# Kernel optimization log

Hardware: AMD Instinct MI355X
Metric: run time of the kernel (lower is better)

## Reference

```python
import jax, jax.numpy as jnp
import numpy as np

B, N, P2, D, L, K = 256, 256, 64, 128, 2, 9  # batch, nodes, patch^2, embed_dim, vig blocks, knn edges
FFN = 4 * D


def _ln(x, g, b, eps=1e-5):
    m = jnp.mean(x, -1, keepdims=True)
    v = jnp.mean((x - m) ** 2, -1, keepdims=True)
    return (x - m) / jnp.sqrt(v + eps) * g + b


def _lrelu(x):
    return jnp.where(x >= 0, x, 0.01 * x)


def _vig_block(x, mask, mf, fc1_w, fc1_b, conv_w, conv_b, fc2_w, fc2_b, f1_w, f1_b, f2_w, f2_b):
    # Grapher: fc1 -> dynamic kNN -> max-relative graph conv -> fc2, residual
    sc = x
    h = x @ fc1_w + fc1_b  # [B,N,D]
    # pairwise squared distances in feature space; masked nodes excluded as neighbors
    x2 = jnp.sum(h * h, -1)
    d2 = x2[:, :, None] + x2[:, None, :] - 2.0 * jnp.einsum('bnd,bmd->bnm', h, h)
    d2 = jnp.where(mask[:, None, :], d2, 1e10)
    _, idx = jax.lax.top_k(-d2, K)  # [B,N,K] nearest-neighbor indices (non-diff)
    Bq, Nq, Dq = h.shape
    hj = jnp.take_along_axis(h, idx.reshape(Bq, Nq * K, 1), axis=1).reshape(Bq, Nq, K, Dq)
    vj = jnp.take_along_axis(mask, idx.reshape(Bq, Nq * K), axis=1).reshape(Bq, Nq, K)
    rel = jnp.where(vj[..., None], hj - h[:, :, None, :], -1e9)
    mrel = jnp.where(vj.any(2)[..., None], rel.max(2), 0.0)  # max-relative aggregation
    h = _lrelu(jnp.concatenate([h, mrel], -1) @ conv_w + conv_b)
    x = (h @ fc2_w + fc2_b) + sc
    # FFN, residual (drop_path = identity at eval)
    sc = x
    x = _lrelu(x @ f1_w + f1_b) @ f2_w + f2_b + sc
    return x * mf


def setup_inputs() -> dict:
    key = jax.random.key(0)
    ks = jax.random.split(key, 32)
    s = 0.02
    d = {
        'nodes_batch': jax.random.normal(ks[0], (B, N, P2), jnp.float32),
        'node_mask': jax.random.randint(ks[1], (B, N), 0, 2) > 0,
        'emb_w1': jax.random.normal(ks[2], (P2, 2 * D), jnp.float32) * s,
        'emb_b1': jnp.zeros((2 * D,), jnp.float32),
        'emb_ln1_g': jnp.ones((2 * D,), jnp.float32),
        'emb_ln1_b': jnp.zeros((2 * D,), jnp.float32),
        'emb_w2': jax.random.normal(ks[3], (2 * D, D), jnp.float32) * s,
        'emb_b2': jnp.zeros((D,), jnp.float32),
        'emb_ln2_g': jnp.ones((D,), jnp.float32),
        'emb_ln2_b': jnp.zeros((D,), jnp.float32),
        'vig_fc1_w': jax.random.normal(ks[4], (L, D, D), jnp.float32) * s,
        'vig_fc1_b': jnp.zeros((L, D), jnp.float32),
        'vig_conv_w': jax.random.normal(ks[5], (L, 2 * D, D), jnp.float32) * s,
        'vig_conv_b': jnp.zeros((L, D), jnp.float32),
        'vig_fc2_w': jax.random.normal(ks[6], (L, D, D), jnp.float32) * s,
        'vig_fc2_b': jnp.zeros((L, D), jnp.float32),
        'vig_ffn1_w': jax.random.normal(ks[7], (L, D, FFN), jnp.float32) * s,
        'vig_ffn1_b': jnp.zeros((L, FFN), jnp.float32),
        'vig_ffn2_w': jax.random.normal(ks[8], (L, FFN, D), jnp.float32) * s,
        'vig_ffn2_b': jnp.zeros((L, D), jnp.float32),
        'out_w1': jax.random.normal(ks[9], (D, 512), jnp.float32) * s,
        'out_b1': jnp.zeros((512,), jnp.float32),
        'out_w2': jax.random.normal(ks[10], (512, 2048), jnp.float32) * s,
        'out_b2': jnp.zeros((2048,), jnp.float32),
    }
    return d


def reference(nodes_batch, node_mask, emb_w1, emb_b1, emb_ln1_g, emb_ln1_b, emb_w2, emb_b2,
              emb_ln2_g, emb_ln2_b, vig_fc1_w, vig_fc1_b, vig_conv_w, vig_conv_b,
              vig_fc2_w, vig_fc2_b, vig_ffn1_w, vig_ffn1_b, vig_ffn2_w, vig_ffn2_b,
              out_w1, out_b1, out_w2, out_b2):
    mf = node_mask[..., None].astype(nodes_batch.dtype)  # [B,N,1]
    # node embed MLP
    x = _lrelu(_ln(nodes_batch @ emb_w1 + emb_b1, emb_ln1_g, emb_ln1_b))
    x = _ln(x @ emb_w2 + emb_b2, emb_ln2_g, emb_ln2_b)
    x = x * mf
    for l in range(L):
        x = _vig_block(x, node_mask, mf,
                       vig_fc1_w[l], vig_fc1_b[l], vig_conv_w[l], vig_conv_b[l],
                       vig_fc2_w[l], vig_fc2_b[l], vig_ffn1_w[l], vig_ffn1_b[l],
                       vig_ffn2_w[l], vig_ffn2_b[l])
    # masked mean pool
    sum_feat = (x * mf).sum(1)
    num_feat = jnp.maximum(mf.sum(1), 1.0)
    g = sum_feat / num_feat
    return _lrelu(g @ out_w1 + out_b1) @ out_w2 + out_b2
```

## Files before the change

### kernel.cpp

```cpp
#include <hip/hip_runtime.h>
#include <cstdint>

#define BB    256
#define NNODE 256
#define PP2   64
#define DD    128
#define LLAY  2
#define KNN   9
#define FFND  512
#define BNROWS (BB*NNODE)

#define LRELU_(v) ((v) >= 0.f ? (v) : 0.01f*(v))

enum { ACT_NONE = 0, ACT_LRELU = 1 };

typedef short  short8_t  __attribute__((ext_vector_type(8)));
typedef float  f32x4     __attribute__((ext_vector_type(4)));
typedef unsigned short us4 __attribute__((ext_vector_type(4)));
typedef unsigned short us8 __attribute__((ext_vector_type(8)));

__device__ inline unsigned short f2bf(float x) {
    unsigned u = __float_as_uint(x);
    unsigned r = (u + 0x7FFFu + ((u >> 16) & 1u)) >> 16;
    return (unsigned short)r;
}
__device__ inline float bf2f(unsigned short h) {
    return __uint_as_float(((unsigned)h) << 16);
}

__device__ inline void gload16(const void* src, void* dst) {
    __builtin_amdgcn_global_load_lds(
        (const __attribute__((address_space(1))) void*)src,
        (__attribute__((address_space(3))) void*)dst, 16, 0, 0);
}

template<int ROWS, int WAVES>
__device__ inline void stage64g(const unsigned short* __restrict__ g, size_t rowbase,
                                int Kel, int k0, unsigned short* lds, int w, int lane)
{
    constexpr int PER = (ROWS*128/1024) / WAVES;
    #pragma unroll
    for (int i = 0; i < PER; ++i) {
        const int inst = w + i*WAVES;
        const unsigned o  = (unsigned)inst*1024u + (unsigned)lane*16u;
        const int      r  = (int)(o >> 7);
        const unsigned cb = o & 127u;
        const unsigned cs = cb ^ ((unsigned)(r & 7) << 4);
        gload16((const char*)(g + (rowbase + (size_t)r)*(size_t)Kel + k0) + cs,
                (char*)lds + (size_t)inst*1024u);
    }
}

__device__ inline short8_t frag64(const unsigned short* lds, int r, int cb) {
    return *reinterpret_cast<const short8_t*>(
        (const char*)lds + (size_t)r*128 + (unsigned)(cb ^ ((r & 7) << 4)));
}

__device__ inline us8 read8sw(const unsigned short* lds, int r, unsigned cb) {
    return *reinterpret_cast<const us8*>(
        (const char*)lds + (size_t)r*128 + (cb ^ ((unsigned)(r & 7) << 4)));
}

__device__ inline unsigned grp16_min_u32(unsigned v) {
    unsigned t;
    t = (unsigned)__builtin_amdgcn_update_dpp(-1, (int)v, 0xB1,  0xF, 0xF, false); v = t < v ? t : v;
    t = (unsigned)__builtin_amdgcn_update_dpp(-1, (int)v, 0x4E,  0xF, 0xF, false); v = t < v ? t : v;
    t = (unsigned)__builtin_amdgcn_update_dpp(-1, (int)v, 0x124, 0xF, 0xF, false); v = t < v ? t : v;
    t = (unsigned)__builtin_amdgcn_update_dpp(-1, (int)v, 0x128, 0xF, 0xF, false); v = t < v ? t : v;
    return v;
}

__device__ inline float dpp_rowsum16(float v) {
    float t;
    t = __uint_as_float((unsigned)__builtin_amdgcn_update_dpp(0, (int)__float_as_uint(v), 0x111, 0xF, 0xF, false)); v += t;
    t = __uint_as_float((unsigned)__builtin_amdgcn_update_dpp(0, (int)__float_as_uint(v), 0x112, 0xF, 0xF, false)); v += t;
    t = __uint_as_float((unsigned)__builtin_amdgcn_update_dpp(0, (int)__float_as_uint(v), 0x114, 0xF, 0xF, false)); v += t;
    t = __uint_as_float((unsigned)__builtin_amdgcn_update_dpp(0, (int)__float_as_uint(v), 0x118, 0xF, 0xF, false)); v += t;
    return v;
}

#define WAITB0  { asm volatile("s_waitcnt vmcnt(0)" ::: "memory");  __builtin_amdgcn_s_barrier(); asm volatile("" ::: "memory"); }
#define WAITB2  { asm volatile("s_waitcnt vmcnt(2)" ::: "memory");  __builtin_amdgcn_s_barrier(); asm volatile("" ::: "memory"); }
#define WAITB3  { asm volatile("s_waitcnt vmcnt(3)" ::: "memory");  __builtin_amdgcn_s_barrier(); asm volatile("" ::: "memory"); }
#define WAITB2L { asm volatile("s_waitcnt vmcnt(2) lgkmcnt(0)" ::: "memory"); __builtin_amdgcn_s_barrier(); asm volatile("" ::: "memory"); }

template<int ACT, bool RES, bool MASK, bool OUTF, bool OUTB, bool OUTS>
__global__ __launch_bounds__(256)
void bgemm_k(const unsigned short* __restrict__ A,
             const unsigned short* __restrict__ W,
             const float* __restrict__ bias,
             const float* __restrict__ resp,
             const int* __restrict__ mask,
             float* __restrict__ Cf, unsigned short* __restrict__ Cb,
             unsigned short* Ohi, unsigned short* Olo,
             int M, int N, int K)
{
    __shared__ __align__(16) unsigned short As[128*64];
    __shared__ __align__(16) unsigned short Bs[128*64];

    const int tid  = threadIdx.x;
    const int lane = tid & 63;
    const int w    = tid >> 6;
    const int wr   = w >> 1, wc = w & 1;
    const int row0 = blockIdx.x * 128;
    const int col0 = blockIdx.y * 128;
    const int l15  = lane & 15;
    const int ko   = lane >> 4;

    f32x4 acc[4][4];
    #pragma unroll
    for (int m = 0; m < 4; ++m)
        #pragma unroll
        for (int n = 0; n < 4; ++n) acc[m][n] = (f32x4){0.f,0.f,0.f,0.f};

    for (int k0 = 0; k0 < K; k0 += 64) {
        stage64g<128,4>(A, (size_t)row0, K, k0, As, w, lane);
        stage64g<128,4>(W, (size_t)col0, K, k0, Bs, w, lane);
        __syncthreads();
        #pragma unroll
        for (int ks = 0; ks < 2; ++ks) {
            short8_t aF[4], bF[4];
            #pragma unroll
            for (int m = 0; m < 4; ++m)
                aF[m] = frag64(As, wr*64 + m*16 + l15, ks*64 + ko*16);
            #pragma unroll
            for (int n = 0; n < 4; ++n)
                bF[n] = frag64(Bs, wc*64 + n*16 + l15, ks*64 + ko*16);
            #pragma unroll
            for (int m = 0; m < 4; ++m)
                #pragma unroll
                for (int n = 0; n < 4; ++n)
                    acc[m][n] = __builtin_amdgcn_mfma_f32_16x16x32_bf16(aF[m], bF[n], acc[m][n], 0, 0, 0);
        }
        __syncthreads();
    }

    #pragma unroll
    for (int m = 0; m < 4; ++m) {
        const int rbase = row0 + wr*64 + m*16 + ko*4;
        #pragma unroll
        for (int n = 0; n < 4; ++n) {
            const int col = col0 + wc*64 + n*16 + l15;
            const float bv = bias[col];
            #pragma unroll
            for (int r = 0; r < 4; ++r) {
                const int row = rbase + r;
                float v = acc[m][n][r] + bv;
                if constexpr (ACT == ACT_LRELU) v = LRELU_(v);
                if constexpr (RES)  v += resp[(size_t)row*N + col];
                if constexpr (MASK) v *= (mask[row] != 0) ? 1.f : 0.f;
                if constexpr (OUTF) Cf[(size_t)row*N + col] = v;
                if constexpr (OUTB) Cb[(size_t)row*N + col] = f2bf(v);
                if constexpr (OUTS) {
                    unsigned short h = f2bf(v);
                    Ohi[(size_t)row*N + col] = h;
                    Olo[(size_t)row*N + col] = f2bf(v - bf2f(h));
                }
            }
        }
    }
}

template<int WR, int WC, bool DO_LRELU, bool MASKMUL, int MODE, bool AF32>
__global__ __launch_bounds__(WR*WC*64)
void bgemm_ln_k(const void* __restrict__ Ap,
                const unsigned short* __restrict__ W,
                const float* __restrict__ bias,
// ... 63 lines not shown
            for (int n = 0; n < 4; ++n)
                bF[n] = frag64(Bs, wc*64 + n*16 + l15, ks*64 + ko*16);
            #pragma unroll
            for (int m = 0; m < 4; ++m)
                #pragma unroll
                for (int n = 0; n < 4; ++n)
                    acc[m][n] = __builtin_amdgcn_mfma_f32_16x16x32_bf16(aF[m], bF[n], acc[m][n], 0, 0, 0);
        }
        __syncthreads();
    }

    float bv[4];
    #pragma unroll
    for (int n = 0; n < 4; ++n) bv[n] = bias[wc*64 + n*16 + l15];
    #pragma unroll
    for (int m = 0; m < 4; ++m)
        #pragma unroll
        for (int n = 0; n < 4; ++n)
            #pragma unroll
            for (int r = 0; r < 4; ++r) acc[m][n][r] += bv[n];

    #pragma unroll
    for (int m = 0; m < 4; ++m) {
        #pragma unroll
        for (int r = 0; r < 4; ++r) {
            float s = acc[m][0][r] + acc[m][1][r] + acc[m][2][r] + acc[m][3][r];
            float q = acc[m][0][r]*acc[m][0][r] + acc[m][1][r]*acc[m][1][r]
                    + acc[m][2][r]*acc[m][2][r] + acc[m][3][r]*acc[m][3][r];
            s = dpp_rowsum16(s);
            q = dpp_rowsum16(q);
            if (l15 == 15) {
                int rl = wr*64 + m*16 + ko*4 + r;
                red_s[wc][rl] = s;
                red_q[wc][rl] = q;
            }
        }
    }
    __syncthreads();
    if (tid < BM) {
        float s = 0.f, q = 0.f;
        #pragma unroll
        for (int c2 = 0; c2 < WC; ++c2) { s += red_s[c2][tid]; q += red_q[c2][tid]; }
        float mu  = s * (1.0f/BN);
        float var = q * (1.0f/BN) - mu*mu;
        mu_l[tid] = mu;
        rs_l[tid] = rsqrtf(fmaxf(var, 0.f) + 1e-5f);
    }
    __syncthreads();

    float gm[4], bt[4];
    #pragma unroll
    for (int n = 0; n < 4; ++n) {
        int col = wc*64 + n*16 + l15;
        gm[n] = gam[col]; bt[n] = bet[col];
    }
    #pragma unroll
    for (int m = 0; m < 4; ++m) {
        #pragma unroll
        for (int r = 0; r < 4; ++r) {
            const int rl  = wr*64 + m*16 + ko*4 + r;
            const int row = row0 + rl;
            const float mu = mu_l[rl], rs = rs_l[rl];
            float mf = 1.f;
            if constexpr (MASKMUL) mf = (mask[row] != 0) ? 1.f : 0.f;
            #pragma unroll
            for (int n = 0; n < 4; ++n) {
                const int col = wc*64 + n*16 + l15;
                float y = (acc[m][n][r] - mu) * rs * gm[n] + bt[n];
                if constexpr (DO_LRELU) y = LRELU_(y);
                if constexpr (MASKMUL)  y *= mf;
                if constexpr (MODE == 1) {
                    ((unsigned short*)outv)[(size_t)row*BN + col] = f2bf(y);
                } else {
                    unsigned short h = f2bf(y);
                    ohi[(size_t)row*BN + col] = h;
                    olo[(size_t)row*BN + col] = f2bf(y - bf2f(h));
                }
            }
        }
    }
}

__global__ __launch_bounds__(1024)
void fc1_dist_topk_gather_k(const unsigned short* __restrict__ xhi,
                            const unsigned short* __restrict__ xlo,
                            const unsigned short* __restrict__ Whi,
                            const unsigned short* __restrict__ Wlo,
                            const float* __restrict__ fc1b,
                            const int* __restrict__ mask,
                            unsigned short* __restrict__ cat)
{
    __shared__ __align__(16) unsigned short BUF[4][NNODE*64];
    __shared__ __align__(16) unsigned short Ws[128*64];
    __shared__ float x2s[NNODE];
    __shared__ unsigned char idx_s[NNODE*KNN];
    __shared__ unsigned char msk_s[NNODE];

    const int b    = blockIdx.x;
    const int tid  = threadIdx.x;
    const int lane = tid & 63;
    const int w    = tid >> 6;
    const int l15  = lane & 15;
    const int g    = lane >> 4;

    const unsigned short* Xhi = xhi + (size_t)b*NNODE*DD;
    const unsigned short* Xlo = xlo + (size_t)b*NNODE*DD;
    const int* mkb = mask + b*NNODE;

    stage64g<NNODE,16>(Xhi, 0, DD, 0,  &BUF[0][0], w, lane);
    stage64g<NNODE,16>(Xhi, 0, DD, 64, &BUF[1][0], w, lane);
    stage64g<NNODE,16>(Xlo, 0, DD, 0,  &BUF[2][0], w, lane);
    stage64g<NNODE,16>(Xlo, 0, DD, 64, &BUF[3][0], w, lane);
    if (tid < NNODE) msk_s[tid] = (mkb[tid] != 0) ? 1 : 0;
    __syncthreads();

    const int arow = w*16 + l15;

    f32x4 hacc[8];
    #pragma unroll
    for (int n = 0; n < 8; ++n) hacc[n] = (f32x4){0.f,0.f,0.f,0.f};

    #pragma unroll
    for (int wp = 0; wp < 4; ++wp) {
        const unsigned short* Wsrc = (wp < 2) ? Whi : Wlo;
        const int kt = wp & 1;
        stage64g<128,16>(Wsrc, 0, DD, kt*64, Ws, w, lane);
        __syncthreads();
        const int nAv = (wp < 2) ? 2 : 1;
        for (int av = 0; av < nAv; ++av) {
            const unsigned short* At = (av == 0) ? &BUF[kt][0] : &BUF[2+kt][0];
            #pragma unroll
            for (int ks = 0; ks < 2; ++ks) {
                short8_t aF = frag64(At, arow, ks*64 + g*16);
                #pragma unroll
                for (int n = 0; n < 8; ++n) {
                    short8_t bF = frag64(Ws, n*16 + l15, ks*64 + g*16);
                    hacc[n] = __builtin_amdgcn_mfma_f32_16x16x32_bf16(aF, bF, hacc[n], 0, 0, 0);
                }
            }
        }
        __syncthreads();
    }

    {
        float qr[4] = {0.f, 0.f, 0.f, 0.f};
        #pragma unroll
        for (int n = 0; n < 8; ++n) {
            const int col = n*16 + l15;
            const float bv = fc1b[col];
            const int kt = col >> 6;
            const unsigned bc = (unsigned)((col & 63) * 2);
            #pragma unroll
            for (int r = 0; r < 4; ++r) {
                const int row = w*16 + g*4 + r;
                float v = hacc[n][r] + bv;
                unsigned short hh = f2bf(v);
                unsigned short hl = f2bf(v - bf2f(hh));
                const unsigned off = (unsigned)(row*128) + (bc ^ ((unsigned)(row & 7) << 4));
                *(unsigned short*)((char*)&BUF[kt][0]   + off) = hh;
                *(unsigned short*)((char*)&BUF[2+kt][0] + off) = hl;
                float vv = bf2f(hh) + bf2f(hl);
                qr[r] += vv*vv;
            }
        }
        #pragma unroll
        for (int r = 0; r < 4; ++r) {
            float q = dpp_rowsum16(qr[r]);
            if (l15 == 15) x2s[w*16 + g*4 + r] = q;
        }
    }
    __syncthreads();

    f32x4 acc[16];
    #pragma unroll
    for (int n = 0; n < 16; ++n) acc[n] = (f32x4){0.f,0.f,0.f,0.f};

    __builtin_amdgcn_s_setprio(1);
    #pragma unroll
    for (int kt = 0; kt < 2; ++kt) {
        #pragma unroll
        for (int ks = 0; ks < 2; ++ks) {
            short8_t aH = frag64(&BUF[kt][0],   arow, ks*64 + g*16);
            short8_t aL = frag64(&BUF[2+kt][0], arow, ks*64 + g*16);
            #pragma unroll
            for (int n = 0; n < 16; ++n) {
                int brow = n*16 + l15;
                short8_t bH = frag64(&BUF[kt][0],   brow, ks*64 + g*16);
                short8_t bL = frag64(&BUF[2+kt][0], brow, ks*64 + g*16);
                acc[n] = __builtin_amdgcn_mfma_f32_16x16x32_bf16(aH, bH, acc[n], 0, 0, 0);
                acc[n] = __builtin_amdgcn_mfma_f32_16x16x32_bf16(aL, bH, acc[n], 0, 0, 0);
                acc[n] = __builtin_amdgcn_mfma_f32_16x16x32_bf16(aH, bL, acc[n], 0, 0, 0);
            }
        }
    }
    __builtin_amdgcn_s_setprio(0);

    float x2c[16]; unsigned mk[16];
    #pragma unroll
    for (int n = 0; n < 16; ++n) {
        int col = n*16 + l15;
        x2c[n] = x2s[col];
        mk[n]  = (unsigned)msk_s[col];
    }

    #pragma unroll
    for (int r = 0; r < 4; ++r) {
        const int rb = w*16 + r;
        if ((msk_s[rb] | msk_s[rb+4] | msk_s[rb+8] | msk_s[rb+12]) == 0) continue;
        const int lrow = w*16 + g*4 + r;
        const float x2r = x2s[lrow];
        unsigned key[16];
        #pragma unroll
        for (int n = 0; n < 16; ++n) {
            float v = x2r + x2c[n] - 2.0f*acc[n][r];
            if (!mk[n]) v = 1e10f;
            unsigned u = __float_as_uint(v);
            u = (u & 0x80000000u) ? ~u : (u | 0x80000000u);
            key[n] = (u & 0xFFFFFF00u) | (unsigned)(n*16 + l15);
        }
        for (int it = 0; it < KNN; ++it) {
            unsigned a0 = key[0]  < key[1]  ? key[0]  : key[1];
            unsigned a1 = key[2]  < key[3]  ? key[2]  : key[3];
            unsigned a2 = key[4]  < key[5]  ? key[4]  : key[5];
            unsigned a3 = key[6]  < key[7]  ? key[6]  : key[7];
            unsigned a4 = key[8]  < key[9]  ? key[8]  : key[9];
            unsigned a5 = key[10] < key[11] ? key[10] : key[11];
            unsigned a6 = key[12] < key[13] ? key[12] : key[13];
            unsigned a7 = key[14] < key[15] ? key[14] : key[15];
            unsigned b0 = a0 < a1 ? a0 : a1;
            unsigned b1 = a2 < a3 ? a2 : a3;
            unsigned b2 = a4 < a5 ? a4 : a5;
            unsigned b3 = a6 < a7 ? a6 : a7;
            unsigned c0 = b0 < b1 ? b0 : b1;
            unsigned c1 = b2 < b3 ? b2 : b3;
            unsigned lmin = c0 < c1 ? c0 : c1;
            unsigned gmin = grp16_min_u32(lmin);
            if (l15 == 0) idx_s[lrow*KNN + it] = (unsigned char)(gmin & 0xFFu);
            #pragma unroll
            for (int n = 0; n < 16; ++n)
                if (key[n] == gmin) key[n] = 0xFFFFFFFFu;
        }
    }

    const int gi = lane & 7;
    const unsigned cb = (unsigned)(gi * 16);
    #pragma unroll
    for (int kt = 0; kt < 2; ++kt) {
        #pragma unroll
        for (int p = 0; p < 2; ++p) {
            const int rl = w*16 + p*8 + (lane >> 3);
            us8 h8 = read8sw(&BUF[kt][0],   rl, cb);
            us8 l8 = read8sw(&BUF[2+kt][0], rl, cb);
            float hi[8], m[8];
            #pragma unroll
            for (int d = 0; d < 8; ++d) { hi[d] = bf2f(h8[d]) + bf2f(l8[d]); m[d] = -1e9f; }
            bool any = false;
            #pragma unroll
            for (int q = 0; q < KNN; ++q) {
                int j = idx_s[rl*KNN + q];
                if (msk_s[j]) {
                    any = true;
                    us8 a = read8sw(&BUF[kt][0],   j, cb);
                    us8 o = read8sw(&BUF[2+kt][0], j, cb);
                    #pragma unroll
                    for (int d = 0; d < 8; ++d)
                        m[d] = fmaxf(m[d], bf2f(a[d]) + bf2f(o[d]));
                }
            }
            us8 o1, o2;
            #pragma unroll
            for (int d = 0; d < 8; ++d) {
                o1[d] = f2bf(hi[d]);
                o2[d] = any ? f2bf(m[d] - hi[d]) : (unsigned short)0;
            }
            const size_t rowbase = (size_t)(b*NNODE + rl)*(2*DD);
            const int c0 = kt*64 + gi*8;
            *reinterpret_cast<us8*>(&cat[rowbase + c0])      = o1;
            *reinterpret_cast<us8*>(&cat[rowbase + DD + c0]) = o2;
        }
    }
}

__global__ __launch_bounds__(512, 4)
void conv_ffn_k(const unsigned short* __restrict__ cat,
                const unsigned short* __restrict__ Wc,
                const float* __restrict__ cb,
                const unsigned short* __restrict__ W2c,
                const float* __restrict__ fb,
                const unsigned short* __restrict__ W1,
                const float* __restrict__ b1,
                const unsigned short* __restrict__ W2f,
                const float* __restrict__ b2,
                const int* __restrict__ mask,
                unsigned short* xhi,
                unsigned short* xlo)
{
    __shared__ __align__(16) unsigned short Bs[3][128*64];
    __shared__ __align__(16) unsigned short h2s[2][64*64];
    __shared__ __align__(16) unsigned short Xs[2][64*64];

    const int tid  = threadIdx.x;
    const int lane = tid & 63;
    const int w    = tid >> 6;
    const int row0 = blockIdx.x * 64;
    const int l15  = lane & 15;
    const int ko   = lane >> 4;

    auto issueB = [&](int t) {
        unsigned short* buf = &Bs[t % 3][0];
        if (t < 4)      stage64g<128,8>(Wc,  0, 256, t*64, buf, w, lane);
        else if (t < 6) stage64g<128,8>(W2c, 0, 128, (t-4)*64, buf, w, lane);
        else {
            int c = (t-6) >> 2, j = (t-6) & 3;
            if (j < 2) stage64g<128,8>(W1, (size_t)(c*128), DD, j*64, buf, w, lane);
            else       stage64g<128,8>(W2f, 0, FFND, c*128 + (j-2)*64, buf, w, lane);
        }
    };

    #define MM8(ATILE, BTILE, ACC)                                              \
        { __builtin_amdgcn_s_setprio(1);                                        \
          _Pragma("unroll")                                                     \
          for (int ks = 0; ks < 2; ++ks) {                                      \
            short8_t aF[4], bF;                                                 \
            _Pragma("unroll")                                                   \
            for (int m = 0; m < 4; ++m) aF[m] = frag64(ATILE, m*16 + l15, ks*64 + ko*16); \
            bF = frag64(BTILE, w*16 + l15, ks*64 + ko*16);                      \
            _Pragma("unroll")                                                   \
            for (int m = 0; m < 4; ++m)                                         \
              ACC[m] = __builtin_amdgcn_mfma_f32_16x16x32_bf16(aF[m], bF, ACC[m], 0, 0, 0); } \
          __builtin_amdgcn_s_setprio(0); }

    #define H2WRITE(ACC, BPTR, DST)                                             \
        { const int kt_ = w >> 2;                                               \
          const int col_ = w*16 + l15;                                          \
          const float bv_ = (BPTR)[col_];                                       \
          const unsigned bc_ = (unsigned)(((w & 3)*16 + l15) * 2);              \
          _Pragma("unroll")                                                     \
          for (int m = 0; m < 4; ++m)                                           \
            _Pragma("unroll")                                                   \
            for (int r = 0; r < 4; ++r) {                                       \
              const int row_ = m*16 + ko*4 + r;                                 \
              float v_ = LRELU_(ACC[m][r] + bv_);                               \
              *(unsigned short*)((char*)&(DST)[kt_][0] + row_*128               \
                  + (bc_ ^ ((unsigned)(row_ & 7) << 4))) = f2bf(v_); } }

    stage64g<64,8>(cat, (size_t)row0, 256, 0,  &Xs[0][0], w, lane);
    issueB(0);
    stage64g<64,8>(cat, (size_t)row0, 256, 64, &Xs[1][0], w, lane);
    issueB(1);

    f32x4 accc[4];
    #pragma unroll
    for (int m = 0; m < 4; ++m) accc[m] = (f32x4){0.f,0.f,0.f,0.f};

    WAITB3;
    issueB(2);
    MM8(&Xs[0][0], &Bs[0][0], accc);

    WAITB2;
    stage64g<64,8>(cat, (size_t)row0, 256, 128, &Xs[0][0], w, lane);
    issueB(3);
    MM8(&Xs[1][0], &Bs[1][0], accc);

    WAITB2;
    stage64g<64,8>(cat, (size_t)row0, 256, 192, &Xs[1][0], w, lane);
    issueB(4);
    MM8(&Xs[0][0], &Bs[2][0], accc);

    WAITB2;
    issueB(5);
    MM8(&Xs[1][0], &Bs[0][0], accc);
    H2WRITE(accc, cb, h2s);

    f32x4 accx[4];
    #pragma unroll
    for (int m = 0; m < 4; ++m) accx[m] = (f32x4){0.f,0.f,0.f,0.f};

    WAITB2L;
    issueB(6);
    MM8(&h2s[0][0], &Bs[1][0], accx);

    WAITB2;
    issueB(7);
    MM8(&h2s[1][0], &Bs[2][0], accx);
    float xn[4][4];
    {
        const int kt = w >> 2;
        const int col = w*16 + l15;
        const float bv = fb[col];
        const unsigned bc = (unsigned)(((w & 3)*16 + l15) * 2);
        #pragma unroll
        for (int m = 0; m < 4; ++m) {
            #pragma unroll
            for (int r = 0; r < 4; ++r) {
                const int row = m*16 + ko*4 + r;
                const size_t gix = (size_t)(row0 + row)*DD + col;
                float res = bf2f(xhi[gix]) + bf2f(xlo[gix]);
                float v = accx[m][r] + bv + res;
                xn[m][r] = v;
                *(unsigned short*)((char*)&Xs[kt][0] + row*128
                    + (bc ^ ((unsigned)(row & 7) << 4))) = f2bf(v);
            }
        }
    }

    f32x4 acc2[4];
    #pragma unroll
    for (int m = 0; m < 4; ++m) acc2[m] = (f32x4){0.f,0.f,0.f,0.f};

    #pragma unroll
    for (int c = 0; c < 4; ++c) {
        const int tb = 6 + c*4;
        f32x4 acc1[4];
        #pragma unroll
        for (int m = 0; m < 4; ++m) acc1[m] = (f32x4){0.f,0.f,0.f,0.f};

        if (c == 0) { WAITB2L; } else { WAITB2; }
        if (tb+2 <= 21) issueB(tb+2);
        MM8(&Xs[0][0], &Bs[tb % 3][0], acc1);

        WAITB2;
        if (tb+3 <= 21) issueB(tb+3);
        MM8(&Xs[1][0], &Bs[(tb+1) % 3][0], acc1);
        H2WRITE(acc1, b1 + c*128, h2s);

        WAITB2L;
        if (tb+4 <= 21) issueB(tb+4);
        MM8(&h2s[0][0], &Bs[(tb+2) % 3][0], acc2);

        if (c == 3) { WAITB0; } else { WAITB2; }
        if (tb+5 <= 21) issueB(tb+5);
        MM8(&h2s[1][0], &Bs[(tb+3) % 3][0], acc2);
    }

    {
        const int col = w*16 + l15;
        const float bv = b2[col];
        #pragma unroll
        for (int m = 0; m < 4; ++m) {
            const int rbase = row0 + m*16 + ko*4;
            #pragma unroll
            for (int r = 0; r < 4; ++r) {
                const int row = rbase + r;
                float v = acc2[m][r] + bv + xn[m][r];
                v *= (mask[row] != 0) ? 1.f : 0.f;
                unsigned short h = f2bf(v);
                xhi[(size_t)row*DD + col] = h;
                xlo[(size_t)row*DD + col] = f2bf(v - bf2f(h));
            }
        }
    }
    #undef MM8
    #undef H2WRITE
}

__global__ __launch_bounds__(128)
void pool_k(const unsigned short* __restrict__ xhi, const unsigned short* __restrict__ xlo,
            const int* __restrict__ mask,
            float* __restrict__ g, unsigned short* __restrict__ gbf)
{
    const int b = blockIdx.x, c = threadIdx.x;
    float s = 0.f; int cnt = 0;
    for (int n = 0; n < NNODE; ++n) {
        const size_t ix = ((size_t)b*NNODE + n)*DD + c;
        s += bf2f(xhi[ix]) + bf2f(xlo[ix]);
        cnt += (mask[b*NNODE + n] != 0) ? 1 : 0;
    }
    float v = s / fmaxf((float)cnt, 1.0f);
    g[b*DD + c] = v;
    gbf[b*DD + c] = f2bf(v);
}

__global__ __launch_bounds__(256)
void prep_all_k(const float* __restrict__ emb_w1, const float* __restrict__ emb_w2,
                const float* __restrict__ conv_w, const float* __restrict__ fc2_w,
                const float* __restrict__ f1_w,   const float* __restrict__ f2_w,
                const float* __restrict__ fc1_w,  const float* __restrict__ ow1,
                const float* __restrict__ ow2,
                unsigned short* __restrict__ emb_w1t, unsigned short* __restrict__ emb_w2t,
                unsigned short* __restrict__ conv_wt, unsigned short* __restrict__ fc2_wt,
                unsigned short* __restrict__ ffn1_wt, unsigned short* __restrict__ ffn2_wt,
                unsigned short* __restrict__ fc1_wthi, unsigned short* __restrict__ fc1_wtlo,
                unsigned short* __restrict__ ow1t, unsigned short* __restrict__ ow2t)
{
    __shared__ float tile[32][33];
    const int tx = threadIdx.x & 31, ty = threadIdx.x >> 5;

    int bid = blockIdx.x;
    const float* src = nullptr; unsigned short* dst = nullptr; unsigned short* dlo = nullptr;
    int K = 0, N = 0;
    do {
        if (bid < 16)  { src = emb_w1; dst = emb_w1t; K = 64;  N = 256; break; }  bid -= 16;
        if (bid < 32)  { src = emb_w2; dst = emb_w2t; K = 256; N = 128; break; }  bid -= 32;
        if (bid < 64)  { int l = bid >> 5; bid &= 31;
                         src = conv_w + (size_t)l*256*128; dst = conv_wt + (size_t)l*128*256;
                         K = 256; N = 128; break; }                               bid -= 64;
        if (bid < 32)  { int l = bid >> 4; bid &= 15;
                         src = fc2_w + (size_t)l*128*128; dst = fc2_wt + (size_t)l*128*128;
                         K = 128; N = 128; break; }                               bid -= 32;
        if (bid < 128) { int l = bid >> 6; bid &= 63;
                         src = f1_w + (size_t)l*128*512; dst = ffn1_wt + (size_t)l*512*128;
                         K = 128; N = 512; break; }                               bid -= 128;
        if (bid < 128) { int l = bid >> 6; bid &= 63;
                         src = f2_w + (size_t)l*512*128; dst = ffn2_wt + (size_t)l*128*512;
                         K = 512; N = 128; break; }                               bid -= 128;
        if (bid < 32)  { int l = bid >> 4; bid &= 15;
                         src = fc1_w + (size_t)l*128*128;
                         dst = fc1_wthi + (size_t)l*128*128; dlo = fc1_wtlo + (size_t)l*128*128;
                         K = 128; N = 128; break; }                               bid -= 32;
        if (bid < 64)  { src = ow1; dst = ow1t; K = 128; N = 512; break; }        bid -= 64;
        { src = ow2; dst = ow2t; K = 512; N = 2048; }
    } while (0);

    const int nbx = N / 32;
    const int bx = bid % nbx, by = bid / nbx;
    const int k0 = by*32, n0 = bx*32;

    #pragma unroll
    for (int i = ty; i < 32; i += 8)
        tile[i][tx] = src[(size_t)(k0+i)*N + n0+tx];
    __syncthreads();
    #pragma unroll
    for (int i = ty; i < 32; i += 8) {
        float v = tile[tx][i];
        unsigned short h = f2bf(v);
        dst[(size_t)(n0+i)*K + k0+tx] = h;
        if (dlo) dlo[(size_t)(n0+i)*K + k0+tx] = f2bf(v - bf2f(h));
    }
}

extern "C" void kernel_launch(void* const* d_in, const int* in_sizes, int n_in,
                              void* d_out, int out_size, void* d_ws, size_t ws_size,
                              hipStream_t stream)
{
    const float* nodes  = (const float*)d_in[0];
    const int*   maskp  = (const int*)  d_in[1];
    const float* emb_w1 = (const float*)d_in[2];
    const float* emb_b1 = (const float*)d_in[3];
    const float* ln1_g  = (const float*)d_in[4];
    const float* ln1_b  = (const float*)d_in[5];
    const float* emb_w2 = (const float*)d_in[6];
    const float* emb_b2 = (const float*)d_in[7];
    const float* ln2_g  = (const float*)d_in[8];
    const float* ln2_b  = (const float*)d_in[9];
    const float* fc1_w  = (const float*)d_in[10];
    const float* fc1_b  = (const float*)d_in[11];
    const float* conv_w = (const float*)d_in[12];
    const float* conv_b = (const float*)d_in[13];
    const float* fc2_w  = (const float*)d_in[14];
    const float* fc2_b  = (const float*)d_in[15];
    const float* f1_w   = (const float*)d_in[16];
    const float* f1_b   = (const float*)d_in[17];
    const float* f2_w   = (const float*)d_in[18];
    const float* f2_b   = (const float*)d_in[19];
    const float* ow1    = (const float*)d_in[20];
    const float* ob1    = (const float*)d_in[21];
    const float* ow2    = (const float*)d_in[22];
    const float* ob2    = (const float*)d_in[23];
    float* out = (float*)d_out;

    char* base = (char*)d_ws;
    char*  H   = base + (size_t)BNROWS*DD*4;
    char*  BIG = H + (size_t)BNROWS*DD*4;
    float*          g     = (float*)(BIG + (size_t)BNROWS*2*DD*4);
    unsigned short* g_bf  = (unsigned short*)(g + BB*DD);
    unsigned short* hid2_bf = g_bf + BB*DD;
    unsigned short* wbuf  = hid2_bf + BB*FFND;

    unsigned short* x_hi   = (unsigned short*)H;
    unsigned short* x_lo   = x_hi + (size_t)BNROWS*DD;
    unsigned short* t256_bf= (unsigned short*)base;
    unsigned short* cat_bf = (unsigned short*)BIG;

    unsigned short* emb_w1t  = wbuf;
    unsigned short* emb_w2t  = emb_w1t + 256*64;
    unsigned short* conv_wt  = emb_w2t + 128*256;
    unsigned short* fc2_wt   = conv_wt + 2*128*256;
    unsigned short* ffn1_wt  = fc2_wt  + 2*128*128;
    unsigned short* ffn2_wt  = ffn1_wt + 2*512*128;
    unsigned short* fc1_wthi = ffn2_wt + 2*128*512;
    unsigned short* fc1_wtlo = fc1_wthi + 2*128*128;
    unsigned short* ow1t     = fc1_wtlo + 2*128*128;
    unsigned short* ow2t     = ow1t + 512*128;

    const dim3 blk(256);

    prep_all_k<<<1520, blk, 0, stream>>>(
        emb_w1, emb_w2, conv_w, fc2_w, f1_w, f2_w, fc1_w, ow1, ow2,
        emb_w1t, emb_w2t, conv_wt, fc2_wt, ffn1_wt, ffn2_wt,
        fc1_wthi, fc1_wtlo, ow1t, ow2t);

    bgemm_ln_k<2,4,true,false,1,true>
        <<<dim3(BNROWS/128), dim3(512), 0, stream>>>
        (nodes, emb_w1t, emb_b1, ln1_g, ln1_b, nullptr, t256_bf, nullptr, nullptr, PP2);
    bgemm_ln_k<2,2,false,true,2,false>
        <<<dim3(BNROWS/128), dim3(256), 0, stream>>>
        (t256_bf, emb_w2t, emb_b2, ln2_g, ln2_b, maskp, nullptr, x_hi, x_lo, 2*DD);

    for (int l = 0; l < LLAY; ++l) {
        const float* fc1b = fc1_b + (size_t)l*DD;
        const float* cb   = conv_b + (size_t)l*DD;
        const float* fc2b = fc2_b + (size_t)l*DD;
        const float* b1   = f1_b + (size_t)l*FFND;
        const float* b2   = f2_b + (size_t)l*DD;

        fc1_dist_topk_gather_k<<<dim3(BB), dim3(1024), 0, stream>>>
            (x_hi, x_lo, fc1_wthi + (size_t)l*DD*DD, fc1_wtlo + (size_t)l*DD*DD,
             fc1b, maskp, cat_bf);
        conv_ffn_k<<<dim3(BNROWS/64), dim3(512), 0, stream>>>
            (cat_bf, conv_wt + (size_t)l*DD*2*DD, cb,
             fc2_wt + (size_t)l*DD*DD, fc2b,
             ffn1_wt + (size_t)l*FFND*DD, b1,
             ffn2_wt + (size_t)l*DD*FFND, b2, maskp,
             x_hi, x_lo);
    }

    pool_k<<<BB, 128, 0, stream>>>(x_hi, x_lo, maskp, g, g_bf);
    bgemm_k<ACT_LRELU,false,false,false,true,false>
        <<<dim3(BB/128, 512/128), blk, 0, stream>>>
        (g_bf, ow1t, ob1, nullptr, nullptr, nullptr, hid2_bf, nullptr, nullptr, BB, 512, DD);
    bgemm_k<ACT_NONE,false,false,true,false,false>
        <<<dim3(BB/128, 2048/128), blk, 0, stream>>>
        (hid2_bf, ow2t, ob2, nullptr, nullptr, out, nullptr, nullptr, nullptr, BB, 2048, 512);
}
```

Baseline: 261.7 us.

## Fuse kNN graph stage with conv, fc2 and FFN into one per-graph kernel

```diff
diff --git a/kernel.cpp b/kernel.cpp
--- a/kernel.cpp
+++ b/kernel.cpp
@@ -78,11 +78,6 @@
     t = __uint_as_float((unsigned)__builtin_amdgcn_update_dpp(0, (int)__float_as_uint(v), 0x118, 0xF, 0xF, false)); v += t;
     return v;
 }
-
-#define WAITB0  { asm volatile("s_waitcnt vmcnt(0)" ::: "memory");  __builtin_amdgcn_s_barrier(); asm volatile("" ::: "memory"); }
-#define WAITB2  { asm volatile("s_waitcnt vmcnt(2)" ::: "memory");  __builtin_amdgcn_s_barrier(); asm volatile("" ::: "memory"); }
-#define WAITB3  { asm volatile("s_waitcnt vmcnt(3)" ::: "memory");  __builtin_amdgcn_s_barrier(); asm volatile("" ::: "memory"); }
-#define WAITB2L { asm volatile("s_waitcnt vmcnt(2) lgkmcnt(0)" ::: "memory"); __builtin_amdgcn_s_barrier(); asm volatile("" ::: "memory"); }
 
 template<int ACT, bool RES, bool MASK, bool OUTF, bool OUTB, bool OUTS>
 __global__ __launch_bounds__(256)
@@ -312,13 +307,20 @@
 }
 
 __global__ __launch_bounds__(1024)
-void fc1_dist_topk_gather_k(const unsigned short* __restrict__ xhi,
-                            const unsigned short* __restrict__ xlo,
-                            const unsigned short* __restrict__ Whi,
-                            const unsigned short* __restrict__ Wlo,
-                            const float* __restrict__ fc1b,
-                            const int* __restrict__ mask,
-                            unsigned short* __restrict__ cat)
+void vig_block_k(unsigned short* xhi,
+                 unsigned short* xlo,
+                 const unsigned short* __restrict__ Whi,
+                 const unsigned short* __restrict__ Wlo,
+                 const float* __restrict__ fc1b,
+                 const int* __restrict__ mask,
+                 const unsigned short* __restrict__ Wc,
+                 const float* __restrict__ cbias,
+                 const unsigned short* __restrict__ W2c,
+                 const float* __restrict__ fb,
+                 const unsigned short* __restrict__ W1,
+                 const float* __restrict__ b1,
+                 const unsigned short* __restrict__ W2f,
+                 const float* __restrict__ b2)
 {
     __shared__ __align__(16) unsigned short BUF[4][NNODE*64];
     __shared__ __align__(16) unsigned short Ws[128*64];
@@ -401,287 +403,268 @@
     }
     __syncthreads();
 
-    f32x4 acc[16];
-    #pragma unroll
-    for (int n = 0; n < 16; ++n) acc[n] = (f32x4){0.f,0.f,0.f,0.f};
-
-    __builtin_amdgcn_s_setprio(1);
+    {
+        f32x4 acc[16];
+        #pragma unroll
+        for (int n = 0; n < 16; ++n) acc[n] = (f32x4){0.f,0.f,0.f,0.f};
+
+        __builtin_amdgcn_s_setprio(1);
+        #pragma unroll
+        for (int kt = 0; kt < 2; ++kt) {
+            #pragma unroll
+            for (int ks = 0; ks < 2; ++ks) {
+                short8_t aH = frag64(&BUF[kt][0],   arow, ks*64 + g*16);
+                short8_t aL = frag64(&BUF[2+kt][0], arow, ks*64 + g*16);
+                #pragma unroll
+                for (int n = 0; n < 16; ++n) {
+                    int brow = n*16 + l15;
+                    short8_t bH = frag64(&BUF[kt][0],   brow, ks*64 + g*16);
+                    short8_t bL = frag64(&BUF[2+kt][0], brow, ks*64 + g*16);
+                    acc[n] = __builtin_amdgcn_mfma_f32_16x16x32_bf16(aH, bH, acc[n], 0, 0, 0);
+                    acc[n] = __builtin_amdgcn_mfma_f32_16x16x32_bf16(aL, bH, acc[n], 0, 0, 0);
+                    acc[n] = __builtin_amdgcn_mfma_f32_16x16x32_bf16(aH, bL, acc[n], 0, 0, 0);
+                }
+            }
+        }
+        __builtin_amdgcn_s_setprio(0);
+
+        float x2c[16]; unsigned mk[16];
+        #pragma unroll
+        for (int n = 0; n < 16; ++n) {
+            int col = n*16 + l15;
+            x2c[n] = x2s[col];
+            mk[n]  = (unsigned)msk_s[col];
+        }
+
+        #pragma unroll
+        for (int r = 0; r < 4; ++r) {
+            const int rb = w*16 + r;
+            if ((msk_s[rb] | msk_s[rb+4] | msk_s[rb+8] | msk_s[rb+12]) == 0) continue;
+            const int lrow = w*16 + g*4 + r;
+            const float x2r = x2s[lrow];
+            unsigned key[16];
+            #pragma unroll
+            for (int n = 0; n < 16; ++n) {
+                float v = x2r + x2c[n] - 2.0f*acc[n][r];
+                if (!mk[n]) v = 1e10f;
+                unsigned u = __float_as_uint(v);
+                u = (u & 0x80000000u) ? ~u : (u | 0x80000000u);
+                key[n] = (u & 0xFFFFFF00u) | (unsigned)(n*16 + l15);
+            }
+            for (int it = 0; it < KNN; ++it) {
+                unsigned a0 = key[0]  < key[1]  ? key[0]  : key[1];
+                unsigned a1 = key[2]  < key[3]  ? key[2]  : key[3];
+                unsigned a2 = key[4]  < key[5]  ? key[4]  : key[5];
+                unsigned a3 = key[6]  < key[7]  ? key[6]  : key[7];
+                unsigned a4 = key[8]  < key[9]  ? key[8]  : key[9];
+                unsigned a5 = key[10] < key[11] ? key[10] : key[11];
+                unsigned a6 = key[12] < key[13] ? key[12] : key[13];
+                unsigned a7 = key[14] < key[15] ? key[14] : key[15];
+                unsigned b0 = a0 < a1 ? a0 : a1;
+                unsigned b1_ = a2 < a3 ? a2 : a3;
+                unsigned b2_ = a4 < a5 ? a4 : a5;
+                unsigned b3 = a6 < a7 ? a6 : a7;
+                unsigned c0 = b0 < b1_ ? b0 : b1_;
+                unsigned c1 = b2_ < b3 ? b2_ : b3;
+                unsigned lmin = c0 < c1 ? c0 : c1;
+                unsigned gmin = grp16_min_u32(lmin);
+                if (l15 == 0) idx_s[lrow*KNN + it] = (unsigned char)(gmin & 0xFFu);
+                #pragma unroll
+                for (int n = 0; n < 16; ++n)
+                    if (key[n] == gmin) key[n] = 0xFFFFFFFFu;
+            }
+        }
+    }
+
+    {
+        us8 o2s[2][2];
+        const int gi = lane & 7;
+        const unsigned cb = (unsigned)(gi * 16);
+        #pragma unroll
+        for (int kt = 0; kt < 2; ++kt) {
+            #pragma unroll
+            for (int p = 0; p < 2; ++p) {
+                const int rl = w*16 + p*8 + (lane >> 3);
+                us8 h8 = read8sw(&BUF[kt][0],   rl, cb);
+                us8 l8 = read8sw(&BUF[2+kt][0], rl, cb);
+                float hi[8], m[8];
+                #pragma unroll
+                for (int d = 0; d < 8; ++d) { hi[d] = bf2f(h8[d]) + bf2f(l8[d]); m[d] = -1e9f; }
+                bool any = false;
+                #pragma unroll
+                for (int q = 0; q < KNN; ++q) {
+                    int j = idx_s[rl*KNN + q];
+                    if (msk_s[j]) {
+                        any = true;
+                        us8 a = read8sw(&BUF[kt][0],   j, cb);
+                        us8 o = read8sw(&BUF[2+kt][0], j, cb);
+                        #pragma unroll
+                        for (int d = 0; d < 8; ++d)
+                            m[d] = fmaxf(m[d], bf2f(a[d]) + bf2f(o[d]));
+                    }
+                }
+                #pragma unroll
+                for (int d = 0; d < 8; ++d)
+                    o2s[kt][p][d] = any ? f2bf(m[d] - hi[d]) : (unsigned short)0;
+            }
+        }
+        __syncthreads();
+        #pragma unroll
+        for (int kt = 0; kt < 2; ++kt) {
+            #pragma unroll
+            for (int p = 0; p < 2; ++p) {
+                const int rl = w*16 + p*8 + (lane >> 3);
+                *reinterpret_cast<us8*>((char*)&BUF[2+kt][0] + (size_t)rl*128
+                    + (cb ^ ((unsigned)(rl & 7) << 4))) = o2s[kt][p];
+            }
+        }
+    }
+    __syncthreads();
+
+    f32x4 accc[8];
+    #pragma unroll
+    for (int n = 0; n < 8; ++n) accc[n] = (f32x4){0.f,0.f,0.f,0.f};
+    #pragma unroll
+    for (int kt4 = 0; kt4 < 4; ++kt4) {
+        stage64g<128,16>(Wc, 0, 256, kt4*64, Ws, w, lane);
+        __syncthreads();
+        #pragma unroll
+        for (int ks = 0; ks < 2; ++ks) {
+            short8_t aF = frag64(&BUF[kt4][0], arow, ks*64 + g*16);
+            #pragma unroll
+            for (int n = 0; n < 8; ++n) {
+                short8_t bF = frag64(Ws, n*16 + l15, ks*64 + g*16);
+                accc[n] = __builtin_amdgcn_mfma_f32_16x16x32_bf16(aF, bF, accc[n], 0, 0, 0);
+            }
+        }
+        __syncthreads();
+    }
+
+    #pragma unroll
+    for (int n = 0; n < 8; ++n) {
+        const int col = n*16 + l15;
+        const float bv = cbias[col];
+        const int kt = col >> 6;
+        const unsigned bc = (unsigned)((col & 63) * 2);
+        #pragma unroll
+        for (int r = 0; r < 4; ++r) {
+            const int row = w*16 + g*4 + r;
+            float v = LRELU_(accc[n][r] + bv);
+            *(unsigned short*)((char*)&BUF[kt][0] + row*128
+                + (bc ^ ((unsigned)(row & 7) << 4))) = f2bf(v);
+        }
+    }
+    __syncthreads();
+
+    f32x4 accx[8];
+    #pragma unroll
+    for (int n = 0; n < 8; ++n) accx[n] = (f32x4){0.f,0.f,0.f,0.f};
     #pragma unroll
     for (int kt = 0; kt < 2; ++kt) {
+        stage64g<128,16>(W2c, 0, 128, kt*64, Ws, w, lane);
+        __syncthreads();
         #pragma unroll
         for (int ks = 0; ks < 2; ++ks) {
-            short8_t aH = frag64(&BUF[kt][0],   arow, ks*64 + g*16);
-            short8_t aL = frag64(&BUF[2+kt][0], arow, ks*64 + g*16);
-            #pragma unroll
-            for (int n = 0; n < 16; ++n) {
-                int brow = n*16 + l15;
-                short8_t bH = frag64(&BUF[kt][0],   brow, ks*64 + g*16);
-                short8_t bL = frag64(&BUF[2+kt][0], brow, ks*64 + g*16);
-                acc[n] = __builtin_amdgcn_mfma_f32_16x16x32_bf16(aH, bH, acc[n], 0, 0, 0);
-                acc[n] = __builtin_amdgcn_mfma_f32_16x16x32_bf16(aL, bH, acc[n], 0, 0, 0);
-                acc[n] = __builtin_amdgcn_mfma_f32_16x16x32_bf16(aH, bL, acc[n], 0, 0, 0);
-            }
-        }
-    }
-    __builtin_amdgcn_s_setprio(0);
-
-    float x2c[16]; unsigned mk[16];
-    #pragma unroll
-    for (int n = 0; n < 16; ++n) {
-        int col = n*16 + l15;
-        x2c[n] = x2s[col];
-        mk[n]  = (unsigned)msk_s[col];
-    }
-
-    #pragma unroll
-    for (int r = 0; r < 4; ++r) {
-        const int rb = w*16 + r;
-        if ((msk_s[rb] | msk_s[rb+4] | msk_s[rb+8] | msk_s[rb+12]) == 0) continue;
-        const int lrow = w*16 + g*4 + r;
-        const float x2r = x2s[lrow];
-        unsigned key[16];
-        #pragma unroll
-        for (int n = 0; n < 16; ++n) {
-            float v = x2r + x2c[n] - 2.0f*acc[n][r];
-            if (!mk[n]) v = 1e10f;
-            unsigned u = __float_as_uint(v);
-            u = (u & 0x80000000u) ? ~u : (u | 0x80000000u);
-            key[n] = (u & 0xFFFFFF00u) | (unsigned)(n*16 + l15);
-        }
-        for (int it = 0; it < KNN; ++it) {
-            unsigned a0 = key[0]  < key[1]  ? key[0]  : key[1];
-            unsigned a1 = key[2]  < key[3]  ? key[2]  : key[3];
-            unsigned a2 = key[4]  < key[5]  ? key[4]  : key[5];
-            unsigned a3 = key[6]  < key[7]  ? key[6]  : key[7];
-            unsigned a4 = key[8]  < key[9]  ? key[8]  : key[9];
-            unsigned a5 = key[10] < key[11] ? key[10] : key[11];
-            unsigned a6 = key[12] < key[13] ? key[12] : key[13];
-            unsigned a7 = key[14] < key[15] ? key[14] : key[15];
-            unsigned b0 = a0 < a1 ? a0 : a1;
-            unsigned b1 = a2 < a3 ? a2 : a3;
-            unsigned b2 = a4 < a5 ? a4 : a5;
-            unsigned b3 = a6 < a7 ? a6 : a7;
-            unsigned c0 = b0 < b1 ? b0 : b1;
-            unsigned c1 = b2 < b3 ? b2 : b3;
-            unsigned lmin = c0 < c1 ? c0 : c1;
-            unsigned gmin = grp16_min_u32(lmin);
-            if (l15 == 0) idx_s[lrow*KNN + it] = (unsigned char)(gmin & 0xFFu);
-            #pragma unroll
-            for (int n = 0; n < 16; ++n)
-                if (key[n] == gmin) key[n] = 0xFFFFFFFFu;
-        }
-    }
-
-    const int gi = lane & 7;
-    const unsigned cb = (unsigned)(gi * 16);
-    #pragma unroll
-    for (int kt = 0; kt < 2; ++kt) {
-        #pragma unroll
-        for (int p = 0; p < 2; ++p) {
-            const int rl = w*16 + p*8 + (lane >> 3);
-            us8 h8 = read8sw(&BUF[kt][0],   rl, cb);
-            us8 l8 = read8sw(&BUF[2+kt][0], rl, cb);
-            float hi[8], m[8];
-            #pragma unroll
-            for (int d = 0; d < 8; ++d) { hi[d] = bf2f(h8[d]) + bf2f(l8[d]); m[d] = -1e9f; }
-            bool any = false;
-            #pragma unroll
-            for (int q = 0; q < KNN; ++q) {
-                int j = idx_s[rl*KNN + q];
-                if (msk_s[j]) {
-                    any = true;
-                    us8 a = read8sw(&BUF[kt][0],   j, cb);
-                    us8 o = read8sw(&BUF[2+kt][0], j, cb);
-                    #pragma unroll
-                    for (int d = 0; d < 8; ++d)
-                        m[d] = fmaxf(m[d], bf2f(a[d]) + bf2f(o[d]));
+            short8_t aF = frag64(&BUF[kt][0], arow, ks*64 + g*16);
+            #pragma unroll
+            for (int n = 0; n < 8; ++n) {
+                short8_t bF = frag64(Ws, n*16 + l15, ks*64 + g*16);
+                accx[n] = __builtin_amdgcn_mfma_f32_16x16x32_bf16(aF, bF, accx[n], 0, 0, 0);
+            }
+        }
+        __syncthreads();
+    }
+
+    float xn[8][4];
+    #pragma unroll
+    for (int n = 0; n < 8; ++n) {
+        const int col = n*16 + l15;
+        const float bv = fb[col];
+        const int kt = col >> 6;
+        const unsigned bc = (unsigned)((col & 63) * 2);
+        #pragma unroll
+        for (int r = 0; r < 4; ++r) {
+            const int row = w*16 + g*4 + r;
+            const size_t gix = (size_t)(b*NNODE + row)*DD + col;
+            float res = bf2f(xhi[gix]) + bf2f(xlo[gix]);
+            float v = accx[n][r] + bv + res;
+            xn[n][r] = v;
+            *(unsigned short*)((char*)&BUF[2+kt][0] + row*128
+                + (bc ^ ((unsigned)(row & 7) << 4))) = f2bf(v);
+        }
+    }
+    __syncthreads();
+
+    f32x4 acc2[8];
+    #pragma unroll
+    for (int n = 0; n < 8; ++n) acc2[n] = (f32x4){0.f,0.f,0.f,0.f};
+
+    for (int c = 0; c < 4; ++c) {
+        f32x4 acc1[8];
+        #pragma unroll
+        for (int n = 0; n < 8; ++n) acc1[n] = (f32x4){0.f,0.f,0.f,0.f};
+        #pragma unroll
+        for (int kt = 0; kt < 2; ++kt) {
+            stage64g<128,16>(W1, (size_t)(c*128), DD, kt*64, Ws, w, lane);
+            __syncthreads();
+            #pragma unroll
+            for (int ks = 0; ks < 2; ++ks) {
+                short8_t aF = frag64(&BUF[2+kt][0], arow, ks*64 + g*16);
+                #pragma unroll
+                for (int n = 0; n < 8; ++n) {
+                    short8_t bF = frag64(Ws, n*16 + l15, ks*64 + g*16);
+                    acc1[n] = __builtin_amdgcn_mfma_f32_16x16x32_bf16(aF, bF, acc1[n], 0, 0, 0);
                 }
             }
-            us8 o1, o2;
-            #pragma unroll
-            for (int d = 0; d < 8; ++d) {
-                o1[d] = f2bf(hi[d]);
-                o2[d] = any ? f2bf(m[d] - hi[d]) : (unsigned short)0;
-            }
-            const size_t rowbase = (size_t)(b*NNODE + rl)*(2*DD);
-            const int c0 = kt*64 + gi*8;
-            *reinterpret_cast<us8*>(&cat[rowbase + c0])      = o1;
-            *reinterpret_cast<us8*>(&cat[rowbase + DD + c0]) = o2;
-        }
-    }
-}
-
-__global__ __launch_bounds__(512, 4)
-void conv_ffn_k(const unsigned short* __restrict__ cat,
-                const unsigned short* __restrict__ Wc,
-                const float* __restrict__ cb,
-                const unsigned short* __restrict__ W2c,
-                const float* __restrict__ fb,
-                const unsigned short* __restrict__ W1,
-                const float* __restrict__ b1,
-                const unsigned short* __restrict__ W2f,
-                const float* __restrict__ b2,
-                const int* __restrict__ mask,
-                unsigned short* xhi,
-                unsigned short* xlo)
-{
-    __shared__ __align__(16) unsigned short Bs[3][128*64];
-    __shared__ __align__(16) unsigned short h2s[2][64*64];
-    __shared__ __align__(16) unsigned short Xs[2][64*64];
-
-    const int tid  = threadIdx.x;
-    const int lane = tid & 63;
-    const int w    = tid >> 6;
-    const int row0 = blockIdx.x * 64;
-    const int l15  = lane & 15;
-    const int ko   = lane >> 4;
-
-    auto issueB = [&](int t) {
-        unsigned short* buf = &Bs[t % 3][0];
-        if (t < 4)      stage64g<128,8>(Wc,  0, 256, t*64, buf, w, lane);
-        else if (t < 6) stage64g<128,8>(W2c, 0, 128, (t-4)*64, buf, w, lane);
-        else {
-            int c = (t-6) >> 2, j = (t-6) & 3;
-            if (j < 2) stage64g<128,8>(W1, (size_t)(c*128), DD, j*64, buf, w, lane);
-            else       stage64g<128,8>(W2f, 0, FFND, c*128 + (j-2)*64, buf, w, lane);
-        }
-    };
-
-    #define MM8(ATILE, BTILE, ACC)                                              \
-        { __builtin_amdgcn_s_setprio(1);                                        \
-          _Pragma("unroll")                                                     \
-          for (int ks = 0; ks < 2; ++ks) {                                      \
-            short8_t aF[4], bF;                                                 \
-            _Pragma("unroll")                                                   \
-            for (int m = 0; m < 4; ++m) aF[m] = frag64(ATILE, m*16 + l15, ks*64 + ko*16); \
-            bF = frag64(BTILE, w*16 + l15, ks*64 + ko*16);                      \
-            _Pragma("unroll")                                                   \
-            for (int m = 0; m < 4; ++m)                                         \
-              ACC[m] = __builtin_amdgcn_mfma_f32_16x16x32_bf16(aF[m], bF, ACC[m], 0, 0, 0); } \
-          __builtin_amdgcn_s_setprio(0); }
-
-    #define H2WRITE(ACC, BPTR, DST)                                             \
-        { const int kt_ = w >> 2;                                               \
-          const int col_ = w*16 + l15;                                          \
-          const float bv_ = (BPTR)[col_];                                       \
-          const unsigned bc_ = (unsigned)(((w & 3)*16 + l15) * 2);              \
-          _Pragma("unroll")                                                     \
-          for (int m = 0; m < 4; ++m)                                           \
-            _Pragma("unroll")                                                   \
-            for (int r = 0; r < 4; ++r) {                                       \
-              const int row_ = m*16 + ko*4 + r;                                 \
-              float v_ = LRELU_(ACC[m][r] + bv_);                               \
-              *(unsigned short*)((char*)&(DST)[kt_][0] + row_*128               \
-                  + (bc_ ^ ((unsigned)(row_ & 7) << 4))) = f2bf(v_); } }
-
-    stage64g<64,8>(cat, (size_t)row0, 256, 0,  &Xs[0][0], w, lane);
-    issueB(0);
-    stage64g<64,8>(cat, (size_t)row0, 256, 64, &Xs[1][0], w, lane);
-    issueB(1);
-
-    f32x4 accc[4];
-    #pragma unroll
-    for (int m = 0; m < 4; ++m) accc[m] = (f32x4){0.f,0.f,0.f,0.f};
-
-    WAITB3;
-    issueB(2);
-    MM8(&Xs[0][0], &Bs[0][0], accc);
-
-    WAITB2;
-    stage64g<64,8>(cat, (size_t)row0, 256, 128, &Xs[0][0], w, lane);
-    issueB(3);
-    MM8(&Xs[1][0], &Bs[1][0], accc);
-
-    WAITB2;
-    stage64g<64,8>(cat, (size_t)row0, 256, 192, &Xs[1][0], w, lane);
-    issueB(4);
-    MM8(&Xs[0][0], &Bs[2][0], accc);
-
-    WAITB2;
-    issueB(5);
-    MM8(&Xs[1][0], &Bs[0][0], accc);
-    H2WRITE(accc, cb, h2s);
-
-    f32x4 accx[4];
-    #pragma unroll
-    for (int m = 0; m < 4; ++m) accx[m] = (f32x4){0.f,0.f,0.f,0.f};
-
-    WAITB2L;
-    issueB(6);
-    MM8(&h2s[0][0], &Bs[1][0], accx);
-
-    WAITB2;
-    issueB(7);
-    MM8(&h2s[1][0], &Bs[2][0], accx);
-    float xn[4][4];
-    {
-        const int kt = w >> 2;
-        const int col = w*16 + l15;
-        const float bv = fb[col];
-        const unsigned bc = (unsigned)(((w & 3)*16 + l15) * 2);
-        #pragma unroll
-        for (int m = 0; m < 4; ++m) {
+            __syncthreads();
+        }
+        #pragma unroll
+        for (int n = 0; n < 8; ++n) {
+            const int col = n*16 + l15;
+            const float bv = b1[c*128 + col];
+            const int kt = col >> 6;
+            const unsigned bc = (unsigned)((col & 63) * 2);
             #pragma unroll
             for (int r = 0; r < 4; ++r) {
-                const int row = m*16 + ko*4 + r;
-                const size_t gix = (size_t)(row0 + row)*DD + col;
-                float res = bf2f(xhi[gix]) + bf2f(xlo[gix]);
-                float v = accx[m][r] + bv + res;
-                xn[m][r] = v;
-                *(unsigned short*)((char*)&Xs[kt][0] + row*128
+                const int row = w*16 + g*4 + r;
+                float v = LRELU_(acc1[n][r] + bv);
+                *(unsigned short*)((char*)&BUF[kt][0] + row*128
                     + (bc ^ ((unsigned)(row & 7) << 4))) = f2bf(v);
             }
         }
-    }
-
-    f32x4 acc2[4];
-    #pragma unroll
-    for (int m = 0; m < 4; ++m) acc2[m] = (f32x4){0.f,0.f,0.f,0.f};
-
-    #pragma unroll
-    for (int c = 0; c < 4; ++c) {
-        const int tb = 6 + c*4;
-        f32x4 acc1[4];
-        #pragma unroll
-        for (int m = 0; m < 4; ++m) acc1[m] = (f32x4){0.f,0.f,0.f,0.f};
-
-        if (c == 0) { WAITB2L; } else { WAITB2; }
-        if (tb+2 <= 21) issueB(tb+2);
-        MM8(&Xs[0][0], &Bs[tb % 3][0], acc1);
-
-        WAITB2;
-        if (tb+3 <= 21) issueB(tb+3);
-        MM8(&Xs[1][0], &Bs[(tb+1) % 3][0], acc1);
-        H2WRITE(acc1, b1 + c*128, h2s);
-
-        WAITB2L;
-        if (tb+4 <= 21) issueB(tb+4);
-        MM8(&h2s[0][0], &Bs[(tb+2) % 3][0], acc2);
-
-        if (c == 3) { WAITB0; } else { WAITB2; }
-        if (tb+5 <= 21) issueB(tb+5);
-        MM8(&h2s[1][0], &Bs[(tb+3) % 3][0], acc2);
-    }
-
-    {
-        const int col = w*16 + l15;
+        __syncthreads();
+        #pragma unroll
+        for (int kt = 0; kt < 2; ++kt) {
+            stage64g<128,16>(W2f, 0, FFND, c*128 + kt*64, Ws, w, lane);
+            __syncthreads();
+            #pragma unroll
+            for (int ks = 0; ks < 2; ++ks) {
+                short8_t aF = frag64(&BUF[kt][0], arow, ks*64 + g*16);
+                #pragma unroll
+                for (int n = 0; n < 8; ++n) {
+                    short8_t bF = frag64(Ws, n*16 + l15, ks*64 + g*16);
+                    acc2[n] = __builtin_amdgcn_mfma_f32_16x16x32_bf16(aF, bF, acc2[n], 0, 0, 0);
+                }
+            }
+            __syncthreads();
+        }
+    }
+
+    #pragma unroll
+    for (int n = 0; n < 8; ++n) {
+        const int col = n*16 + l15;
         const float bv = b2[col];
         #pragma unroll
-        for (int m = 0; m < 4; ++m) {
-            const int rbase = row0 + m*16 + ko*4;
-            #pragma unroll
-            for (int r = 0; r < 4; ++r) {
-                const int row = rbase + r;
-                float v = acc2[m][r] + bv + xn[m][r];
-                v *= (mask[row] != 0) ? 1.f : 0.f;
-                unsigned short h = f2bf(v);
-                xhi[(size_t)row*DD + col] = h;
-                xlo[(size_t)row*DD + col] = f2bf(v - bf2f(h));
-            }
-        }
-    }
-    #undef MM8
-    #undef H2WRITE
+        for (int r = 0; r < 4; ++r) {
+            const int row = w*16 + g*4 + r;
+            const size_t gix = (size_t)(b*NNODE + row)*DD + col;
+            float v = acc2[n][r] + bv + xn[n][r];
+            v *= msk_s[row] ? 1.f : 0.f;
+            unsigned short h = f2bf(v);
+            xhi[gix] = h;
+            xlo[gix] = f2bf(v - bf2f(h));
+        }
+    }
 }
 
 __global__ __launch_bounds__(128)
@@ -800,7 +783,6 @@
     unsigned short* x_hi   = (unsigned short*)H;
     unsigned short* x_lo   = x_hi + (size_t)BNROWS*DD;
     unsigned short* t256_bf= (unsigned short*)base;
-    unsigned short* cat_bf = (unsigned short*)BIG;
 
     unsigned short* emb_w1t  = wbuf;
     unsigned short* emb_w2t  = emb_w1t + 256*64;
@@ -828,21 +810,14 @@
         (t256_bf, emb_w2t, emb_b2, ln2_g, ln2_b, maskp, nullptr, x_hi, x_lo, 2*DD);
 
     for (int l = 0; l < LLAY; ++l) {
-        const float* fc1b = fc1_b + (size_t)l*DD;
-        const float* cb   = conv_b + (size_t)l*DD;
-        const float* fc2b = fc2_b + (size_t)l*DD;
-        const float* b1   = f1_b + (size_t)l*FFND;
-        const float* b2   = f2_b + (size_t)l*DD;
-
-        fc1_dist_topk_gather_k<<<dim3(BB), dim3(1024), 0, stream>>>
-            (x_hi, x_lo, fc1_wthi + (size_t)l*DD*DD, fc1_wtlo + (size_t)l*DD*DD,
-             fc1b, maskp, cat_bf);
-        conv_ffn_k<<<dim3(BNROWS/64), dim3(512), 0, stream>>>
-            (cat_bf, conv_wt + (size_t)l*DD*2*DD, cb,
-             fc2_wt + (size_t)l*DD*DD, fc2b,
-             ffn1_wt + (size_t)l*FFND*DD, b1,
-             ffn2_wt + (size_t)l*DD*FFND, b2, maskp,
-             x_hi, x_lo);
+        vig_block_k<<<dim3(BB), dim3(1024), 0, stream>>>
+            (x_hi, x_lo,
+             fc1_wthi + (size_t)l*DD*DD, fc1_wtlo + (size_t)l*DD*DD,
+             fc1_b + (size_t)l*DD, maskp,
+             conv_wt + (size_t)l*DD*2*DD, conv_b + (size_t)l*DD,
+             fc2_wt + (size_t)l*DD*DD,   fc2_b + (size_t)l*DD,
+             ffn1_wt + (size_t)l*FFND*DD, f1_b + (size_t)l*FFND,
+             ffn2_wt + (size_t)l*DD*FFND, f2_b + (size_t)l*DD);
     }
 
     pool_k<<<BB, 128, 0, stream>>>(x_hi, x_lo, maskp, g, g_bf);
```

Result: slower. 320.6 us (+22.5%).
